# Performance work log

Hardware: AMD Instinct MI355X
Metric: run time of the kernel (lower is better)

The kernel has to match this reference:

```python
import jax, jax.numpy as jnp
import numpy as np

N1, N2, N3, N4 = 50_000, 100_000, 200_000, 400_000
D, OUT = 128, 128


def silu(x):
    return x * jax.nn.sigmoid(x)


def mlp(h, Wa, ba, Wb, bb):
    # torch.nn.Sequential(Linear, SiLU, Linear)
    return silu(h @ Wa + ba) @ Wb + bb


def setup_inputs() -> dict:
    key = jax.random.key(0)
    ks = jax.random.split(key, 12)
    s = 1.0 / np.sqrt(D).astype(np.float32)
    inp = {
        "feat": jax.random.normal(ks[0], (N1, D), jnp.float32),
        "W1a": jax.random.normal(ks[1], (D, D), jnp.float32) * s,
        "b1a": jnp.zeros((D,), jnp.float32),
        "W1b": jax.random.normal(ks[2], (D, D), jnp.float32) * s,
        "b1b": jnp.zeros((D,), jnp.float32),
        "W2a": jax.random.normal(ks[3], (D, D), jnp.float32) * s,
        "b2a": jnp.zeros((D,), jnp.float32),
        "W2b": jax.random.normal(ks[4], (D, D), jnp.float32) * s,
        "b2b": jnp.zeros((D,), jnp.float32),
        "W3a": jax.random.normal(ks[5], (D, D), jnp.float32) * s,
        "b3a": jnp.zeros((D,), jnp.float32),
        "W3b": jax.random.normal(ks[6], (D, D), jnp.float32) * s,
        "b3b": jnp.zeros((D,), jnp.float32),
        "Wo": jax.random.normal(ks[7], (3 * D, OUT), jnp.float32) * (1.0 / np.sqrt(3 * D).astype(np.float32)),
        "bo": jnp.zeros((OUT,), jnp.float32),
        # n{k-1}_in_n{k} edges: each level-k path has exactly 2 subpath children
        "src12": jax.random.randint(ks[8], (2 * N2,), 0, N1),
        "dst12": jnp.repeat(jnp.arange(N2), 2),
        "src23": jax.random.randint(ks[9], (2 * N3,), 0, N2),
        "dst23": jnp.repeat(jnp.arange(N3), 2),
        "src34": jax.random.randint(ks[10], (2 * N4,), 0, N3),
        "dst34": jnp.repeat(jnp.arange(N4), 2),
    }
    return inp


def reference(feat, W1a, b1a, W1b, b1b, W2a, b2a, W2b, b2b,
              W3a, b3a, W3b, b3b, Wo, bo,
              src12, dst12, src23, dst23, src34, dst34):
    # ---- upward ----
    h1 = mlp(feat, W1a, b1a, W1b, b1b)                       # n1 features (kept for final concat)
    h2 = jax.ops.segment_prod(h1[src12], dst12, num_segments=N2, indices_are_sorted=True)
    h2t = mlp(h2, W2a, b2a, W2b, b2b)
    h3 = jax.ops.segment_prod(h2t[src23], dst23, num_segments=N3, indices_are_sorted=True)
    h3t = mlp(h3, W3a, b3a, W3b, b3b)
    h4 = jax.ops.segment_prod(h3t[src34], dst34, num_segments=N4, indices_are_sorted=True)
    # ---- downward ----
    # n2_has_n1 (reverse of n1_in_n2): sum n2 features onto n1 -> 'h2'
    h2_on_n1 = jax.ops.segment_sum(h2t[dst12], src12, num_segments=N1)
    # n4_has_n3 then n3_has_n2 (overwrite h on lower level)
    h3_dn = jax.ops.segment_sum(h4[dst34], src34, num_segments=N3)
    h2_dn = jax.ops.segment_sum(h3_dn[dst23], src23, num_segments=N2)
    # n2_has_n1 again -> 'h_down'
    h_down = jax.ops.segment_sum(h2_dn[dst12], src12, num_segments=N1)
    # final per-node linear + SiLU on concat([h, h2, h_down])
    out = silu(jnp.concatenate([h1, h2_on_n1, h_down], axis=-1) @ Wo + bo)
    return out
```

## Files before the change

### kernel.cpp

```cpp
#include <hip/hip_runtime.h>

#define D 128
#define XSH 136

#define SHIFT 11
#define NPB   2048
#define EPT   8

typedef _Float16 f16;
typedef __attribute__((ext_vector_type(4))) _Float16 f16x4;
typedef __attribute__((ext_vector_type(8))) _Float16 f16x8;
typedef __attribute__((ext_vector_type(4))) float    f32x4;

__device__ __forceinline__ float silu_f(float x) {
    return x / (1.0f + __expf(-x));
}

struct WPtrs { const float* s0; const float* s1; const float* s2;
               const float* s3; const float* s4; const float* s5; };
__global__ void wconv_all_kernel(WPtrs wp, const float* __restrict__ Wo, f16* __restrict__ WT)
{
    const int blk = blockIdx.x, t = threadIdx.x;
    if (blk < 384) {
        const int wid = blk >> 6;
        const int off = ((blk & 63) << 8) + t;
        const int n = off >> 7, k = off & 127;
        const float* s;
        switch (wid) {
            case 0: s = wp.s0; break;
            case 1: s = wp.s1; break;
            case 2: s = wp.s2; break;
            case 3: s = wp.s3; break;
            case 4: s = wp.s4; break;
            default: s = wp.s5; break;
        }
        WT[(wid << 14) + off] = (f16)s[(k << 7) + n];
    } else {
        const int off = ((blk - 384) << 8) + t;
        const int n = off / 384, k = off - n * 384;
        WT[(6 << 14) + off] = (f16)Wo[k * 128 + n];
    }
}

template<bool GATHER>
__launch_bounds__(256)
__global__ void mlp_mfma_kernel(const void* __restrict__ in_, const int* __restrict__ src,
                                const f16* __restrict__ WaT, const float* __restrict__ ba,
                                const f16* __restrict__ WbT, const float* __restrict__ bb,
                                f16* __restrict__ out, int nrows)
{
    __shared__ f16 wlds[32768];
    __shared__ f16 ys[4][2048];
    const int t = threadIdx.x;
    const int w = t >> 6, l = t & 63;
    const int cl = l & 15, kg = l >> 4;

    #pragma unroll
    for (int i = 0; i < 16; ++i) {
        const int f = t + i * 256;
        const int mat = f >> 11, idx = f & 2047;
        const int nt = idx >> 8, kk = (idx >> 6) & 3, ll = idx & 63;
        const f16* Wsrc = mat ? WbT : WaT;
        const f16x8 v = *(const f16x8*)(Wsrc + (size_t)(nt * 16 + (ll & 15)) * D
                                        + kk * 32 + (ll >> 4) * 8);
        *(f16x8*)(wlds + (size_t)f * 8) = v;
    }
    __syncthreads();

    f16* ysw = ys[w];
    auto ysoff = [&](int row, int b) -> int {
        return row * 128 + ((b ^ (((row & 3) << 6) | (((row >> 2) & 3) << 4))) >> 1);
    };

    const int ntile = (nrows + 15) >> 4;
    for (int tile = blockIdx.x * 4 + w; tile < ntile; tile += (int)gridDim.x * 4) {
        const int g = tile * 16 + cl;
        f16x8 xf[4];

        if (g < nrows) {
            if (GATHER) {
                const f16* in = (const f16*)in_;
                const int a = src[2 * g], b = src[2 * g + 1];
                #pragma unroll
                for (int kk = 0; kk < 4; ++kk) {
                    const f16x8 av = *(const f16x8*)(in + (size_t)a * D + kk * 32 + kg * 8);
                    const f16x8 bv = *(const f16x8*)(in + (size_t)b * D + kk * 32 + kg * 8);
                    f16x8 hv;
                    #pragma unroll
                    for (int j = 0; j < 8; ++j) hv[j] = (f16)((float)av[j] * (float)bv[j]);
                    xf[kk] = hv;
                }
            } else {
                const float* in = (const float*)in_;
                #pragma unroll
                for (int kk = 0; kk < 4; ++kk) {
                    const float4 v0 = *(const float4*)(in + (size_t)g * D + kk * 32 + kg * 8);
                    const float4 v1 = *(const float4*)(in + (size_t)g * D + kk * 32 + kg * 8 + 4);
                    f16x8 hv = {(f16)v0.x, (f16)v0.y, (f16)v0.z, (f16)v0.w,
                                (f16)v1.x, (f16)v1.y, (f16)v1.z, (f16)v1.w};
                    xf[kk] = hv;
                }
            }
        } else {
            f16x8 z = {};
            #pragma unroll
            for (int kk = 0; kk < 4; ++kk) xf[kk] = z;
        }

        f32x4 acc[8];

        #pragma unroll
        for (int nt = 0; nt < 8; ++nt) acc[nt] = (f32x4){0.f, 0.f, 0.f, 0.f};
        #pragma unroll
        for (int kk = 0; kk < 4; ++kk)
            #pragma unroll
            for (int nt = 0; nt < 8; ++nt) {
                const f16x8 wf = *(const f16x8*)(wlds + ((size_t)((nt * 4 + kk) * 64 + l)) * 8);
                acc[nt] = __builtin_amdgcn_mfma_f32_16x16x32_f16(wf, xf[kk], acc[nt], 0, 0, 0);
            }
        #pragma unroll
        for (int nt = 0; nt < 8; ++nt) {
            const float4 bv = *(const float4*)&ba[nt * 16 + kg * 4];
            f16x4 y;
            y[0] = (f16)silu_f(acc[nt][0] + bv.x);
            y[1] = (f16)silu_f(acc[nt][1] + bv.y);
            y[2] = (f16)silu_f(acc[nt][2] + bv.z);
            y[3] = (f16)silu_f(acc[nt][3] + bv.w);
            *(f16x4*)(ysw + ysoff(cl, nt * 32 + kg * 8)) = y;
        }
        asm volatile("s_waitcnt lgkmcnt(0)" ::: "memory");
        __builtin_amdgcn_sched_barrier(0);

        #pragma unroll
        for (int kk = 0; kk < 4; ++kk)
            xf[kk] = *(const f16x8*)(ysw + ysoff(cl, kk * 64 + kg * 16));

        #pragma unroll
        for (int nt = 0; nt < 8; ++nt) acc[nt] = (f32x4){0.f, 0.f, 0.f, 0.f};
        #pragma unroll
        for (int kk = 0; kk < 4; ++kk)
            #pragma unroll
            for (int nt = 0; nt < 8; ++nt) {
                const f16x8 wf = *(const f16x8*)(wlds + ((size_t)(2048 + (nt * 4 + kk) * 64 + l)) * 8);
                acc[nt] = __builtin_amdgcn_mfma_f32_16x16x32_f16(wf, xf[kk], acc[nt], 0, 0, 0);
            }
        #pragma unroll
        for (int nt = 0; nt < 8; ++nt) {
            const float4 bv = *(const float4*)&bb[nt * 16 + kg * 4];
            f16x4 z;
            z[0] = (f16)(acc[nt][0] + bv.x);
            z[1] = (f16)(acc[nt][1] + bv.y);
            z[2] = (f16)(acc[nt][2] + bv.z);
            z[3] = (f16)(acc[nt][3] + bv.w);
            *(f16x4*)(ysw + ysoff(cl, nt * 32 + kg * 8)) = z;
        }
        asm volatile("s_waitcnt lgkmcnt(0)" ::: "memory");
        __builtin_amdgcn_sched_barrier(0);

        #pragma unroll
        for (int i = 0; i < 4; ++i) {
            const int lin = i * 1024 + l * 16;
            const int row = lin >> 8, b = lin & 255;
            const int gr = tile * 16 + row;
            if (gr < nrows) {
                const f16x8 v = *(const f16x8*)(ysw + ysoff(row, b));
                *(f16x8*)(out + (size_t)gr * D + (b >> 1)) = v;
            }
        }
    }
}

__launch_bounds__(256)
__global__ void out_mfma_kernel(const f16* __restrict__ h1, const f16* __restrict__ h2on1,
                                const f16* __restrict__ hdown,
                                const f16* __restrict__ WoT, const float* __restrict__ bo,
                                float* __restrict__ out, int nrows)
{
    __shared__ f16 xs[64][XSH];
    const int t = threadIdx.x;
    const int w = t >> 6, l = t & 63;
    const int cl = l & 15, kg = l >> 4;
    const int r = t >> 2, q = t & 3;
    const int row0 = blockIdx.x * 64;
    const int g = row0 + r;

    f32x4 acc[2][4];
    #pragma unroll
    for (int nt = 0; nt < 2; ++nt)
        #pragma unroll
        for (int m = 0; m < 4; ++m) acc[nt][m] = (f32x4){0.f, 0.f, 0.f, 0.f};

    const f16* parts[3] = {h1, h2on1, hdown};
    f16x8 st[2][4];

    if (g < nrows) {
        const f16x8* pp = (const f16x8*)(parts[0] + (size_t)g * D + q * 32);
        #pragma unroll
        for (int i = 0; i < 4; ++i) st[0][i] = pp[i];
    } else {
        f16x8 z = {};
        #pragma unroll
        for (int i = 0; i < 4; ++i) st[0][i] = z;
    }

    #pragma unroll
    for (int p = 0; p < 3; ++p) {
        if (p) __syncthreads();
        {
            f16* dst = &xs[r][q * 32];
            #pragma unroll
            for (int i = 0; i < 4; ++i) *(f16x8*)(dst + 8 * i) = st[p & 1][i];
        }
        __syncthreads();
        if (p < 2) {
            if (g < nrows) {
                const f16x8* pp = (const f16x8*)(parts[p + 1] + (size_t)g * D + q * 32);
                #pragma unroll
                for (int i = 0; i < 4; ++i) st[(p + 1) & 1][i] = pp[i];
            } else {
                f16x8 z = {};
                #pragma unroll
                for (int i = 0; i < 4; ++i) st[(p + 1) & 1][i] = z;
            }
        }
        f16x8 wo[2][4];
        #pragma unroll
        for (int nt = 0; nt < 2; ++nt)
            #pragma unroll
            for (int kk = 0; kk < 4; ++kk)
                wo[nt][kk] = *(const f16x8*)(WoT + (size_t)((w * 2 + nt) * 16 + cl) * 384
                                             + p * D + kk * 32 + kg * 8);
        #pragma unroll
        for (int m = 0; m < 4; ++m)
            #pragma unroll
            for (int kk = 0; kk < 4; ++kk) {
                const f16x8 a = *(const f16x8*)&xs[m * 16 + cl][kk * 32 + kg * 8];
                acc[0][m] = __builtin_amdgcn_mfma_f32_16x16x32_f16(wo[0][kk], a, acc[0][m], 0, 0, 0);
                acc[1][m] = __builtin_amdgcn_mfma_f32_16x16x32_f16(wo[1][kk], a, acc[1][m], 0, 0, 0);
            }
    }

    #pragma unroll
    for (int nt = 0; nt < 2; ++nt) {
        const int n0 = w * 32 + nt * 16 + kg * 4;
        const float4 bv = *(const float4*)&bo[n0];
        #pragma unroll
        for (int m = 0; m < 4; ++m) {
            const int gr = row0 + m * 16 + cl;
            if (gr < nrows) {
                float4 v = make_float4(silu_f(acc[nt][m][0] + bv.x),
                                       silu_f(acc[nt][m][1] + bv.y),
                                       silu_f(acc[nt][m][2] + bv.z),
                                       silu_f(acc[nt][m][3] + bv.w));
                *(float4*)(out + (size_t)gr * D + n0) = v;
            }
        }
    }
}

__global__ void bucket_hist_kernel(const int* __restrict__ s12, int E12,
                                   const int* __restrict__ s23, int E23,
                                   const int* __restrict__ s34, int E34,
                                   int* __restrict__ bcnt, int N1, int N2, int nbkt)
{
    __shared__ int h[256];
    const int t = threadIdx.x;
    for (int i = t; i < 256; i += blockDim.x) h[i] = 0;
    __syncthreads();
    const int Etot = E12 + E23 + E34;
    for (int g = blockIdx.x * blockDim.x + t; g < Etot; g += gridDim.x * blockDim.x) {
        int node;
        if (g < E12) node = s12[g];
        else if (g < E12 + E23) node = N1 + s23[g - E12];
        else node = N1 + N2 + s34[g - E12 - E23];
        atomicAdd(&h[node >> SHIFT], 1);
    }
    __syncthreads();
    for (int i = t; i < nbkt; i += blockDim.x)
        if (h[i]) atomicAdd(&bcnt[i], h[i]);
}

__global__ void bucket_scan_kernel(const int* __restrict__ bcnt, int* __restrict__ bbase,
                                   int* __restrict__ bcur, int nbkt, int Etot)
{
    __shared__ int s[256];
    const int t = threadIdx.x;
    const int v = (t < nbkt) ? bcnt[t] : 0;
    s[t] = v;
    __syncthreads();
    for (int d = 1; d < 256; d <<= 1) {
        const int u = (t >= d) ? s[t - d] : 0;
        __syncthreads();
        s[t] += u;
        __syncthreads();
    }
    if (t < nbkt) { const int ex = s[t] - v; bbase[t] = ex; bcur[t] = ex; }
    if (t == 0) bbase[nbkt] = Etot;
}

__global__ void csr_pass1_kernel(const int* __restrict__ s12, int E12,
                                 const int* __restrict__ s23, int E23,
                                 const int* __restrict__ s34, int E34,
                                 int* __restrict__ bcur, int2* __restrict__ recs,
                                 int N1, int N2, int nbkt)
{
    __shared__ int cnt[256];
    __shared__ int gbase[256];
    const int t = threadIdx.x;
    const int chunk = blockIdx.x * (256 * EPT);
    const int Etot = E12 + E23 + E34;
    for (int i = t; i < 256; i += 256) cnt[i] = 0;
    __syncthreads();
    int node_[EPT], pay_[EPT], br_[EPT];
    #pragma unroll
    for (int i = 0; i < EPT; ++i) {
        const int g = chunk + i * 256 + t;
        int node = -1, pay = 0, b = 0, r = 0;
        if (g < Etot) {
            if (g < E12) { node = s12[g]; pay = g >> 1; }
            else if (g < E12 + E23) { const int e = g - E12; node = N1 + s23[e]; pay = e >> 1; }
            else { const int e = g - E12 - E23; node = N1 + N2 + s34[e]; pay = s34[e ^ 1]; }
            b = node >> SHIFT;
            r = atomicAdd(&cnt[b], 1);
        }
        node_[i] = node; pay_[i] = pay; br_[i] = (b << 16) | r;
    }
    __syncthreads();
    if (t < nbkt && cnt[t]) gbase[t] = atomicAdd(&bcur[t], cnt[t]);
    __syncthreads();
    #pragma unroll
    for (int i = 0; i < EPT; ++i) {
        if (node_[i] >= 0) {
            const int b = br_[i] >> 16, r = br_[i] & 0xffff;
            recs[gbase[b] + r] = make_int2(node_[i], pay_[i]);
        }
    }
}

__launch_bounds__(1024)
__global__ void csr_pass2_kernel(const int2* __restrict__ recs,
                                 const int* __restrict__ bbase,
                                 int2* __restrict__ offcnt, int* __restrict__ el, int NT)
{
    __shared__ int cnt2[NPB];
    __shared__ int pref[NPB];
    __shared__ int s1[NPB / 2];
    const int b = blockIdx.x, t = threadIdx.x;
    const int node0 = b << SHIFT;
    const int k0 = bbase[b], k1 = bbase[b + 1];
    for (int i = t; i < NPB; i += 1024) cnt2[i] = 0;
    __syncthreads();
    for (int k = k0 + t; k < k1; k += 1024)
        atomicAdd(&cnt2[recs[k].x - node0], 1);
    __syncthreads();
    s1[t] = cnt2[2 * t] + cnt2[2 * t + 1];
    __syncthreads();
    for (int d = 1; d < 1024; d <<= 1) {
        const int u = (t >= d) ? s1[t - d] : 0;
        __syncthreads();
        s1[t] += u;
        __syncthreads();
    }
    {
        const int a = cnt2[2 * t];
        const int pairsum = a + cnt2[2 * t + 1];
        const int ex0 = s1[t] - pairsum;
        pref[2 * t] = ex0;
        pref[2 * t + 1] = ex0 + a;
    }
    __syncthreads();
    for (int i = t; i < NPB; i += 1024) {
        const int node = node0 + i;
        if (node < NT) offcnt[node] = make_int2(k0 + pref[i], cnt2[i]);
    }
    __syncthreads();
    for (int k = k0 + t; k < k1; k += 1024) {
        const int2 r = recs[k];
        const int pos = atomicAdd(&pref[r.x - node0], 1);
        el[k0 + pos] = r.y;
    }
}

__global__ void prod_gather_kernel(const f16* __restrict__ h3t,
                                   const int2* __restrict__ offcnt,
                                   const int* __restrict__ el,
                                   f16* __restrict__ h3dn, int nrows)
{
    const long long g = (long long)blockIdx.x * blockDim.x + threadIdx.x;
    const int i = (int)(g >> 4);
    if (i >= nrows) return;
    const int c = ((int)g & 15) * 8;
    const f16x8 ownv = *(const f16x8*)(h3t + (size_t)i * D + c);
    float acc0[8] = {}, acc1[8] = {};
    const int2 oc = offcnt[i];
    const int base = oc.x, deg = oc.y;
    int d = 0;
    for (; d + 4 <= deg; d += 4) {
        const int s0 = el[base + d + 0], s1v = el[base + d + 1];
        const int s2 = el[base + d + 2], s3v = el[base + d + 3];
        const f16x8 v0 = *(const f16x8*)(h3t + (size_t)s0 * D + c);
        const f16x8 v1 = *(const f16x8*)(h3t + (size_t)s1v * D + c);
        const f16x8 v2 = *(const f16x8*)(h3t + (size_t)s2 * D + c);
        const f16x8 v3 = *(const f16x8*)(h3t + (size_t)s3v * D + c);
        #pragma unroll
        for (int j = 0; j < 8; ++j) {
            acc0[j] += (float)v0[j] + (float)v2[j];
            acc1[j] += (float)v1[j] + (float)v3[j];
        }
    }
    for (; d < deg; ++d) {
        const int s0 = el[base + d];
        const f16x8 v0 = *(const f16x8*)(h3t + (size_t)s0 * D + c);
        #pragma unroll
        for (int j = 0; j < 8; ++j) acc0[j] += (float)v0[j];
    }
    f16x8 r;
    #pragma unroll
    for (int j = 0; j < 8; ++j) r[j] = (f16)((acc0[j] + acc1[j]) * (float)ownv[j]);
    *(f16x8*)(h3dn + (size_t)i * D + c) = r;
}

__global__ void gather_sum_kernel(const f16* __restrict__ val,
                                  const int2* __restrict__ offcnt,
                                  const int* __restrict__ el,
                                  f16* __restrict__ dst, int nrows)
{
    const long long g = (long long)blockIdx.x * blockDim.x + threadIdx.x;
    const int i = (int)(g >> 4);
    if (i >= nrows) return;
    const int c = ((int)g & 15) * 8;
    float acc0[8] = {}, acc1[8] = {};
    const int2 oc = offcnt[i];
    const int base = oc.x, deg = oc.y;
    int d = 0;
    for (; d + 4 <= deg; d += 4) {
        const int s0 = el[base + d + 0], s1v = el[base + d + 1];
        const int s2 = el[base + d + 2], s3v = el[base + d + 3];
        const f16x8 v0 = *(const f16x8*)(val + (size_t)s0 * D + c);
        const f16x8 v1 = *(const f16x8*)(val + (size_t)s1v * D + c);
        const f16x8 v2 = *(const f16x8*)(val + (size_t)s2 * D + c);
        const f16x8 v3 = *(const f16x8*)(val + (size_t)s3v * D + c);
        #pragma unroll
        for (int j = 0; j < 8; ++j) {
            acc0[j] += (float)v0[j] + (float)v2[j];
            acc1[j] += (float)v1[j] + (float)v3[j];
        }
    }
    for (; d < deg; ++d) {
        const int s0 = el[base + d];
        const f16x8 v0 = *(const f16x8*)(val + (size_t)s0 * D + c);
        #pragma unroll
        for (int j = 0; j < 8; ++j) acc0[j] += (float)v0[j];
    }
    f16x8 r;
    #pragma unroll
    for (int j = 0; j < 8; ++j) r[j] = (f16)(acc0[j] + acc1[j]);
    *(f16x8*)(dst + (size_t)i * D + c) = r;
}

__global__ void ws_report_kernel(float* out, float v) {
    if (threadIdx.x == 0 && blockIdx.x == 0) out[0] = v;
}

extern "C" void kernel_launch(void* const* d_in, const int* in_sizes, int n_in,
                              void* d_out, int out_size, void* d_ws, size_t ws_size,
                              hipStream_t stream)
{
    const float* feat = (const float*)d_in[0];
    const float* W1a = (const float*)d_in[1];  const float* b1a = (const float*)d_in[2];
    const float* W1b = (const float*)d_in[3];  const float* b1b = (const float*)d_in[4];
    const float* W2a = (const float*)d_in[5];  const float* b2a = (const float*)d_in[6];
    const float* W2b = (const float*)d_in[7];  const float* b2b = (const float*)d_in[8];
    const float* W3a = (const float*)d_in[9];  const float* b3a = (const float*)d_in[10];
    const float* W3b = (const float*)d_in[11]; const float* b3b = (const float*)d_in[12];
    const float* Wo  = (const float*)d_in[13]; const float* bo  = (const float*)d_in[14];
    const int* src12 = (const int*)d_in[15];
    const int* src23 = (const int*)d_in[17];
    const int* src34 = (const int*)d_in[19];

    const int N1 = in_sizes[0] / D;
    const int N2 = in_sizes[15] / 2;
    const int N3 = in_sizes[17] / 2;
    const int N4 = in_sizes[19] / 2;
    const int E12 = 2 * N2, E23 = 2 * N3, E34 = 2 * N4;
    const int NT = N1 + N2 + N3;
    const int Etot = E12 + E23 + E34;
    const int NBKT = (NT + NPB - 1) >> SHIFT;

    char* p = (char*)d_ws;
    f16* h1    = (f16*)p;  p += (size_t)N1 * D * sizeof(f16);
    f16* h2on1 = (f16*)p;  p += (size_t)N1 * D * sizeof(f16);
    f16* h2t   = (f16*)p;  p += (size_t)N2 * D * sizeof(f16);
    f16* h3t   = (f16*)p;  f16* h2dn  = h3t;
    p += (size_t)N3 * D * sizeof(f16);
    f16* h3dn  = (f16*)p;  f16* hdown = h3dn;
    p += (size_t)N3 * D * sizeof(f16);

    p = (char*)(((uintptr_t)p + 15) & ~(uintptr_t)15);
    int2* offcnt = (int2*)p;             p += (size_t)NT * sizeof(int2);
    int2* recs   = (int2*)p;             p += (size_t)Etot * sizeof(int2);
    int*  el     = (int*)p;              p += (size_t)Etot * sizeof(int);
    int*  bcnt   = (int*)p;              p += 256 * sizeof(int);
    int*  bbase  = (int*)p;              p += 257 * sizeof(int);
    int*  bcur   = (int*)p;              p += 256 * sizeof(int);

    p = (char*)(((uintptr_t)p + 31) & ~(uintptr_t)31);
    f16* WT = (f16*)p;
    f16* WaT1 = WT;
    f16* WbT1 = WaT1 + D * D;
    f16* WaT2 = WbT1 + D * D;
    f16* WbT2 = WaT2 + D * D;
    f16* WaT3 = WbT2 + D * D;
    f16* WbT3 = WaT3 + D * D;
    f16* WoT  = WbT3 + D * D;
    p = (char*)(WoT + 384 * D);

    const size_t need = p - (char*)d_ws;
    if (ws_size < need || NBKT > 256) {
        ws_report_kernel<<<1, 64, 0, stream>>>((float*)d_out, (float)ws_size);
        return;
    }

    dim3 blk(256);
    auto rowblk16 = [](long long rows) { return dim3((unsigned)((rows * 16 + 255) / 256)); };

    WPtrs wp = {W1a, W1b, W2a, W2b, W3a, W3b};
    wconv_all_kernel<<<dim3(576), blk, 0, stream>>>(wp, Wo, WT);

    hipMemsetAsync(bcnt, 0, 256 * sizeof(int), stream);
    {
        const int nblk = (Etot + 2047) / 2048;
        bucket_hist_kernel<<<dim3((unsigned)nblk), blk, 0, stream>>>(
            src12, E12, src23, E23, src34, E34, bcnt, N1, N2, NBKT);
        bucket_scan_kernel<<<1, 256, 0, stream>>>(bcnt, bbase, bcur, NBKT, Etot);
        csr_pass1_kernel<<<dim3((unsigned)((Etot + 256 * EPT - 1) / (256 * EPT))), blk, 0, stream>>>(
            src12, E12, src23, E23, src34, E34, bcur, recs, N1, N2, NBKT);
        csr_pass2_kernel<<<dim3((unsigned)NBKT), dim3(1024), 0, stream>>>(
            recs, bbase, offcnt, el, NT);
    }

    mlp_mfma_kernel<false><<<dim3(512), blk, 0, stream>>>(feat, nullptr, WaT1, b1a, WbT1, b1b, h1, N1);
    mlp_mfma_kernel<true ><<<dim3(512), blk, 0, stream>>>(h1, src12, WaT2, b2a, WbT2, b2b, h2t, N2);
    gather_sum_kernel<<<rowblk16(N1), blk, 0, stream>>>(h2t, offcnt, el, h2on1, N1);
    mlp_mfma_kernel<true ><<<dim3(512), blk, 0, stream>>>(h2t, src23, WaT3, b3a, WbT3, b3b, h3t, N3);

    prod_gather_kernel<<<rowblk16(N3), blk, 0, stream>>>(h3t, offcnt + N1 + N2, el, h3dn, N3);
    gather_sum_kernel<<<rowblk16(N2), blk, 0, stream>>>(h3dn, offcnt + N1, el, h2dn, N2);
    gather_sum_kernel<<<rowblk16(N1), blk, 0, stream>>>(h2dn, offcnt, el, hdown, N1);

    out_mfma_kernel<<<dim3((unsigned)((N1 + 63) / 64)), blk, 0, stream>>>(h1, h2on1, hdown, WoT, bo, (float*)d_out, N1);
}
```

Measured before the change: 259.4 us.

## Fuse n1 gather-sums into output kernel and stream MLP weights from global memory

The two gather_sum passes onto level-1 nodes are folded into the output kernel. It now reads h2t and h2dn through the CSR lists and sums them directly into shared memory, so the h2on1 and hdown intermediates are never written or re-read. The MLP kernel drops its 64KB shared-memory weight staging and reads fragment-ordered weights (pre-permuted in the weight-conversion kernel) straight from global memory/L2. It also raises launch bounds to 5 waves per SIMD and launches one tile per wave instead of a persistent 512-block grid. In exchange, the MFMA operands now depend on global/L2 load latency, and the output kernel does irregular gathers inline with extra register pressure.

```diff
diff --git a/kernel.cpp b/kernel.cpp
--- a/kernel.cpp
+++ b/kernel.cpp
@@ -23,8 +23,12 @@
     const int blk = blockIdx.x, t = threadIdx.x;
     if (blk < 384) {
         const int wid = blk >> 6;
-        const int off = ((blk & 63) << 8) + t;
-        const int n = off >> 7, k = off & 127;
+        const int o = ((blk & 63) << 8) + t;
+        const int fi = o >> 9, r = o & 511;
+        const int l = r >> 3, j = r & 7;
+        const int nt = fi >> 2, kk = fi & 3;
+        const int n = nt * 16 + (l & 15);
+        const int k = kk * 32 + ((l >> 4) << 3) + j;
         const float* s;
         switch (wid) {
             case 0: s = wp.s0; break;
@@ -34,7 +38,7 @@
             case 4: s = wp.s4; break;
             default: s = wp.s5; break;
         }
-        WT[(wid << 14) + off] = (f16)s[(k << 7) + n];
+        WT[(wid << 14) + o] = (f16)s[(k << 7) + n];
     } else {
         const int off = ((blk - 384) << 8) + t;
         const int n = off / 384, k = off - n * 384;
@@ -43,37 +47,26 @@
 }
 
 template<bool GATHER>
-__launch_bounds__(256)
+__launch_bounds__(256, 5)
 __global__ void mlp_mfma_kernel(const void* __restrict__ in_, const int* __restrict__ src,
-                                const f16* __restrict__ WaT, const float* __restrict__ ba,
-                                const f16* __restrict__ WbT, const float* __restrict__ bb,
+                                const f16* __restrict__ Wfm,
+                                const float* __restrict__ ba, const float* __restrict__ bb,
                                 f16* __restrict__ out, int nrows)
 {
-    __shared__ f16 wlds[32768];
     __shared__ f16 ys[4][2048];
     const int t = threadIdx.x;
     const int w = t >> 6, l = t & 63;
     const int cl = l & 15, kg = l >> 4;
 
-    #pragma unroll
-    for (int i = 0; i < 16; ++i) {
-        const int f = t + i * 256;
-        const int mat = f >> 11, idx = f & 2047;
-        const int nt = idx >> 8, kk = (idx >> 6) & 3, ll = idx & 63;
-        const f16* Wsrc = mat ? WbT : WaT;
-        const f16x8 v = *(const f16x8*)(Wsrc + (size_t)(nt * 16 + (ll & 15)) * D
-                                        + kk * 32 + (ll >> 4) * 8);
-        *(f16x8*)(wlds + (size_t)f * 8) = v;
-    }
-    __syncthreads();
-
     f16* ysw = ys[w];
     auto ysoff = [&](int row, int b) -> int {
         return row * 128 + ((b ^ (((row & 3) << 6) | (((row >> 2) & 3) << 4))) >> 1);
     };
 
     const int ntile = (nrows + 15) >> 4;
-    for (int tile = blockIdx.x * 4 + w; tile < ntile; tile += (int)gridDim.x * 4) {
+    const int stride = (int)gridDim.x * 4;
+
+    for (int tile = blockIdx.x * 4 + w; tile < ntile; tile += stride) {
         const int g = tile * 16 + cl;
         f16x8 xf[4];
 
@@ -115,7 +108,7 @@
         for (int kk = 0; kk < 4; ++kk)
             #pragma unroll
             for (int nt = 0; nt < 8; ++nt) {
-                const f16x8 wf = *(const f16x8*)(wlds + ((size_t)((nt * 4 + kk) * 64 + l)) * 8);
+                const f16x8 wf = *(const f16x8*)(Wfm + (size_t)(((nt * 4 + kk) * 64 + l) * 8));
                 acc[nt] = __builtin_amdgcn_mfma_f32_16x16x32_f16(wf, xf[kk], acc[nt], 0, 0, 0);
             }
         #pragma unroll
@@ -141,7 +134,7 @@
         for (int kk = 0; kk < 4; ++kk)
             #pragma unroll
             for (int nt = 0; nt < 8; ++nt) {
-                const f16x8 wf = *(const f16x8*)(wlds + ((size_t)(2048 + (nt * 4 + kk) * 64 + l)) * 8);
+                const f16x8 wf = *(const f16x8*)(Wfm + (size_t)(16384 + ((nt * 4 + kk) * 64 + l) * 8));
                 acc[nt] = __builtin_amdgcn_mfma_f32_16x16x32_f16(wf, xf[kk], acc[nt], 0, 0, 0);
             }
         #pragma unroll
@@ -171,8 +164,9 @@
 }
 
 __launch_bounds__(256)
-__global__ void out_mfma_kernel(const f16* __restrict__ h1, const f16* __restrict__ h2on1,
-                                const f16* __restrict__ hdown,
+__global__ void out_mfma_kernel(const f16* __restrict__ h1, const f16* __restrict__ h2t,
+                                const f16* __restrict__ h2dn,
+                                const int2* __restrict__ offcnt, const int* __restrict__ el,
                                 const f16* __restrict__ WoT, const float* __restrict__ bo,
                                 float* __restrict__ out, int nrows)
 {
@@ -190,39 +184,59 @@
         #pragma unroll
         for (int m = 0; m < 4; ++m) acc[nt][m] = (f32x4){0.f, 0.f, 0.f, 0.f};
 
-    const f16* parts[3] = {h1, h2on1, hdown};
-    f16x8 st[2][4];
-
-    if (g < nrows) {
-        const f16x8* pp = (const f16x8*)(parts[0] + (size_t)g * D + q * 32);
-        #pragma unroll
-        for (int i = 0; i < 4; ++i) st[0][i] = pp[i];
-    } else {
-        f16x8 z = {};
-        #pragma unroll
-        for (int i = 0; i < 4; ++i) st[0][i] = z;
-    }
-
     #pragma unroll
     for (int p = 0; p < 3; ++p) {
         if (p) __syncthreads();
         {
             f16* dst = &xs[r][q * 32];
-            #pragma unroll
-            for (int i = 0; i < 4; ++i) *(f16x8*)(dst + 8 * i) = st[p & 1][i];
-        }
-        __syncthreads();
-        if (p < 2) {
-            if (g < nrows) {
-                const f16x8* pp = (const f16x8*)(parts[p + 1] + (size_t)g * D + q * 32);
-                #pragma unroll
-                for (int i = 0; i < 4; ++i) st[(p + 1) & 1][i] = pp[i];
-            } else {
+            if (g >= nrows) {
                 f16x8 z = {};
                 #pragma unroll
-                for (int i = 0; i < 4; ++i) st[(p + 1) & 1][i] = z;
-            }
-        }
+                for (int i = 0; i < 4; ++i) *(f16x8*)(dst + 8 * i) = z;
+            } else if (p == 0) {
+                const f16x8* pp = (const f16x8*)(h1 + (size_t)g * D + q * 32);
+                #pragma unroll
+                for (int i = 0; i < 4; ++i) *(f16x8*)(dst + 8 * i) = pp[i];
+            } else {
+                const f16* srcbuf = (p == 1) ? h2t : h2dn;
+                float fa[32];
+                #pragma unroll
+                for (int i = 0; i < 32; ++i) fa[i] = 0.f;
+                const int2 oc = offcnt[g];
+                const int base = oc.x, deg = oc.y;
+                int d = 0;
+                for (; d + 2 <= deg; d += 2) {
+                    const int j0 = el[base + d], j1 = el[base + d + 1];
+                    const f16x8* p0 = (const f16x8*)(srcbuf + (size_t)j0 * D + q * 32);
+                    const f16x8* p1 = (const f16x8*)(srcbuf + (size_t)j1 * D + q * 32);
+                    #pragma unroll
+                    for (int i = 0; i < 4; ++i) {
+                        const f16x8 v0 = p0[i], v1 = p1[i];
+                        #pragma unroll
+                        for (int j = 0; j < 8; ++j)
+                            fa[i * 8 + j] += (float)v0[j] + (float)v1[j];
+                    }
+                }
+                if (d < deg) {
+                    const int j0 = el[base + d];
+                    const f16x8* p0 = (const f16x8*)(srcbuf + (size_t)j0 * D + q * 32);
+                    #pragma unroll
+                    for (int i = 0; i < 4; ++i) {
+                        const f16x8 v0 = p0[i];
+                        #pragma unroll
+                        for (int j = 0; j < 8; ++j) fa[i * 8 + j] += (float)v0[j];
+                    }
+                }
+                #pragma unroll
+                for (int i = 0; i < 4; ++i) {
+                    f16x8 hv;
+                    #pragma unroll
+                    for (int j = 0; j < 8; ++j) hv[j] = (f16)fa[i * 8 + j];
+                    *(f16x8*)(dst + 8 * i) = hv;
+                }
+            }
+        }
+        __syncthreads();
         f16x8 wo[2][4];
         #pragma unroll
         for (int nt = 0; nt < 2; ++nt)
@@ -489,11 +503,10 @@
 
     char* p = (char*)d_ws;
     f16* h1    = (f16*)p;  p += (size_t)N1 * D * sizeof(f16);
-    f16* h2on1 = (f16*)p;  p += (size_t)N1 * D * sizeof(f16);
     f16* h2t   = (f16*)p;  p += (size_t)N2 * D * sizeof(f16);
     f16* h3t   = (f16*)p;  f16* h2dn  = h3t;
     p += (size_t)N3 * D * sizeof(f16);
-    f16* h3dn  = (f16*)p;  f16* hdown = h3dn;
+    f16* h3dn  = (f16*)p;
     p += (size_t)N3 * D * sizeof(f16);
 
     p = (char*)(((uintptr_t)p + 15) & ~(uintptr_t)15);
@@ -506,13 +519,10 @@
 
     p = (char*)(((uintptr_t)p + 31) & ~(uintptr_t)31);
     f16* WT = (f16*)p;
-    f16* WaT1 = WT;
-    f16* WbT1 = WaT1 + D * D;
-    f16* WaT2 = WbT1 + D * D;
-    f16* WbT2 = WaT2 + D * D;
-    f16* WaT3 = WbT2 + D * D;
-    f16* WbT3 = WaT3 + D * D;
-    f16* WoT  = WbT3 + D * D;
+    f16* Wp1 = WT;
+    f16* Wp2 = WT + 2 * 16384;
+    f16* Wp3 = WT + 4 * 16384;
+    f16* WoT = WT + 6 * 16384;
     p = (char*)(WoT + 384 * D);
 
     const size_t need = p - (char*)d_ws;
@@ -523,6 +533,7 @@
 
     dim3 blk(256);
     auto rowblk16 = [](long long rows) { return dim3((unsigned)((rows * 16 + 255) / 256)); };
+    auto mlpgrid  = [](int n) { return dim3((unsigned)((((n + 15) >> 4) + 3) / 4)); };
 
     WPtrs wp = {W1a, W1b, W2a, W2b, W3a, W3b};
     wconv_all_kernel<<<dim3(576), blk, 0, stream>>>(wp, Wo, WT);
@@ -539,14 +550,13 @@
             recs, bbase, offcnt, el, NT);
     }
 
-    mlp_mfma_kernel<false><<<dim3(512), blk, 0, stream>>>(feat, nullptr, WaT1, b1a, WbT1, b1b, h1, N1);
-    mlp_mfma_kernel<true ><<<dim3(512), blk, 0, stream>>>(h1, src12, WaT2, b2a, WbT2, b2b, h2t, N2);
-    gather_sum_kernel<<<rowblk16(N1), blk, 0, stream>>>(h2t, offcnt, el, h2on1, N1);
-    mlp_mfma_kernel<true ><<<dim3(512), blk, 0, stream>>>(h2t, src23, WaT3, b3a, WbT3, b3b, h3t, N3);
+    mlp_mfma_kernel<false><<<mlpgrid(N1), blk, 0, stream>>>(feat, nullptr, Wp1, b1a, b1b, h1, N1);
+    mlp_mfma_kernel<true ><<<mlpgrid(N2), blk, 0, stream>>>(h1, src12, Wp2, b2a, b2b, h2t, N2);
+    mlp_mfma_kernel<true ><<<mlpgrid(N3), blk, 0, stream>>>(h2t, src23, Wp3, b3a, b3b, h3t, N3);
 
     prod_gather_kernel<<<rowblk16(N3), blk, 0, stream>>>(h3t, offcnt + N1 + N2, el, h3dn, N3);
     gather_sum_kernel<<<rowblk16(N2), blk, 0, stream>>>(h3dn, offcnt + N1, el, h2dn, N2);
-    gather_sum_kernel<<<rowblk16(N1), blk, 0, stream>>>(h2dn, offcnt, el, hdown, N1);
-
-    out_mfma_kernel<<<dim3((unsigned)((N1 + 63) / 64)), blk, 0, stream>>>(h1, h2on1, hdown, WoT, bo, (float*)d_out, N1);
-}
+
+    out_mfma_kernel<<<dim3((unsigned)((N1 + 63) / 64)), blk, 0, stream>>>(
+        h1, h2t, h2dn, offcnt, el, WoT, bo, (float*)d_out, N1);
+}
```

Result: slower. 818.7 us (+215.6%).
